# Performance work log

Measured on AMD Instinct MI355X. Metric: run time of the kernel, lower is better.

Reference implementation:

```python
import jax, jax.numpy as jnp
import numpy as np

N = 50000   # nodes
E = 800000  # edges (avg degree 16)
G = 64      # graphs in batch


def setup_inputs() -> dict:
    key = jax.random.key(0)
    ks = jax.random.split(key, 32)
    w = lambda k, shape, s=0.05: (jax.random.normal(k, shape, jnp.float32) * s)
    inp = {}
    inp["x"] = jax.random.normal(ks[0], (N, 3), jnp.float32)
    inp["edge_index"] = jax.random.randint(ks[1], (2, E), 0, N)
    inp["batch"] = jnp.sort(jax.random.randint(ks[2], (N,), 0, G))
    # TransformerConv 1: in=3, heads=2, d=32 -> out 64 (concat)
    inp["Wq1"] = w(ks[3], (3, 64));  inp["bq1"] = w(ks[4], (64,))
    inp["Wk1"] = w(ks[5], (3, 64));  inp["bk1"] = w(ks[6], (64,))
    inp["Wv1"] = w(ks[7], (3, 64));  inp["bv1"] = w(ks[8], (64,))
    inp["Ws1"] = w(ks[9], (3, 64));  inp["bs1"] = w(ks[10], (64,))
    # TransformerConv 2: in=64, heads=2, d=64 -> out 128 (concat)
    inp["Wq2"] = w(ks[11], (64, 128)); inp["bq2"] = w(ks[12], (128,))
    inp["Wk2"] = w(ks[13], (64, 128)); inp["bk2"] = w(ks[14], (128,))
    inp["Wv2"] = w(ks[15], (64, 128)); inp["bv2"] = w(ks[16], (128,))
    inp["Ws2"] = w(ks[17], (64, 128)); inp["bs2"] = w(ks[18], (128,))
    # MLP head
    inp["W1"] = w(ks[19], (128, 32)); inp["b1"] = w(ks[20], (32,))
    inp["W2"] = w(ks[21], (32, 128)); inp["b2"] = w(ks[22], (128,))
    inp["W3"] = w(ks[23], (128, 40)); inp["b3"] = w(ks[24], (40,))
    return inp


def _transformer_conv(x, src, dst, Wq, bq, Wk, bk, Wv, bv, Ws, bs, H, d):
    """PyG TransformerConv (concat=True, root_weight=True, beta=False)."""
    n = x.shape[0]
    q = (x @ Wq + bq).reshape(n, H, d)
    k = (x @ Wk + bk).reshape(n, H, d)
    v = (x @ Wv + bv).reshape(n, H, d)
    # per-edge attention logits: q_i . k_j / sqrt(d), i=dst, j=src  -> [E, H]
    s = (q[dst] * k[src]).sum(-1) / jnp.sqrt(jnp.float32(d))
    # segment softmax over edges grouped by destination node
    m = jax.ops.segment_max(s, dst, num_segments=n)
    m = jnp.where(jnp.isfinite(m), m, 0.0)
    e = jnp.exp(s - m[dst])
    denom = jax.ops.segment_sum(e, dst, num_segments=n)
    alpha = e / jnp.maximum(denom[dst], 1e-16)
    # scatter-add weighted values
    out = jax.ops.segment_sum(alpha[:, :, None] * v[src], dst, num_segments=n)
    return out.reshape(n, H * d) + x @ Ws + bs  # skip connection


def reference(x, edge_index, batch,
              Wq1, bq1, Wk1, bk1, Wv1, bv1, Ws1, bs1,
              Wq2, bq2, Wk2, bk2, Wv2, bv2, Ws2, bs2,
              W1, b1, W2, b2, W3, b3):
    src, dst = edge_index[0], edge_index[1]
    h = jax.nn.relu(_transformer_conv(x, src, dst, Wq1, bq1, Wk1, bk1,
                                      Wv1, bv1, Ws1, bs1, 2, 32))
    h = jax.nn.relu(_transformer_conv(h, src, dst, Wq2, bq2, Wk2, bk2,
                                      Wv2, bv2, Ws2, bs2, 2, 64))
    # global max pool over graphs
    p = jax.ops.segment_max(h, batch, num_segments=G)
    p = jnp.where(jnp.isfinite(p), p, 0.0)
    x_latent = jax.nn.relu(p @ W1 + b1)
    y = jax.nn.relu(x_latent @ W2 + b2)
    return (y @ W3 + b3, x_latent)
```

## Files before the change

kernel.cpp:

```cpp
#include <hip/hip_runtime.h>
#include <hip/hip_bf16.h>

typedef short s16x8 __attribute__((ext_vector_type(8)));
typedef float f32x4 __attribute__((ext_vector_type(4)));

#define LOG2E 1.4426950408889634f

__device__ __forceinline__ float bfl(unsigned w) { return __uint_as_float(w << 16); }
__device__ __forceinline__ float bfh(unsigned w) { return __uint_as_float(w & 0xffff0000u); }
__device__ __forceinline__ unsigned f2bf(float f) {
    unsigned u = __float_as_uint(f);
    return (u + 0x7fffu + ((u >> 16) & 1u)) >> 16;
}

__global__ void deg_part(const int* __restrict__ dst, int* __restrict__ deg,
                         int E, int rsize) {
    int r = blockIdx.x & 7;
    int e = (blockIdx.x >> 3) * blockDim.x + threadIdx.x;
    if (e < E) {
        int d = dst[e];
        if (d / rsize == r) atomicAdd(&deg[d], 1);
    }
}

__global__ void scan_reduce(const int* __restrict__ deg, int* __restrict__ bsum, int n) {
    __shared__ int sh[256];
    int t = threadIdx.x;
    int i = blockIdx.x * 256 + t;
    sh[t] = (i < n) ? deg[i] : 0;
    __syncthreads();
    for (int s = 128; s > 0; s >>= 1) {
        if (t < s) sh[t] += sh[t + s];
        __syncthreads();
    }
    if (t == 0) bsum[blockIdx.x] = sh[0];
}

__global__ void scan_apply(const int* __restrict__ deg, const int* __restrict__ bsum,
                           int* __restrict__ off, int* __restrict__ cursor,
                           int n, int nb, int Etot) {
    __shared__ int sh[256], sb[256];
    int t = threadIdx.x;
    int b = blockIdx.x;
    sb[t] = (t < nb && t < b) ? bsum[t] : 0;
    int i = b * 256 + t;
    int v = (i < n) ? deg[i] : 0;
    sh[t] = v;
    __syncthreads();
    for (int s = 128; s > 0; s >>= 1) {
        if (t < s) sb[t] += sb[t + s];
        __syncthreads();
    }
    int boffb = sb[0];
    __syncthreads();
    for (int d = 1; d < 256; d <<= 1) {
        int x = (t >= d) ? sh[t - d] : 0;
        __syncthreads();
        sh[t] += x;
        __syncthreads();
    }
    int ex = sh[t] - v + boffb;
    if (i < n) {
        off[i] = ex;
        cursor[i] = ex;
    }
    if (b == 0 && t == 0) off[n] = Etot;
}

__global__ void scatter_part(const int* __restrict__ src, const int* __restrict__ dst,
                             int* __restrict__ cursor, int* __restrict__ srcs,
                             int E, int rsize) {
    int r = blockIdx.x & 7;
    int e = (blockIdx.x >> 3) * blockDim.x + threadIdx.x;
    if (e < E) {
        int d = dst[e];
        if (d / rsize == r) {
            int p = atomicAdd(&cursor[d], 1);
            srcs[p] = src[e];
        }
    }
}

__global__ void prep_all(const float* __restrict__ Wq1, const float* __restrict__ bq1,
                         const float* __restrict__ Wk1,
                         const float* __restrict__ Wq2, const float* __restrict__ bq2,
                         const float* __restrict__ Wk2,
                         const float* __restrict__ Wv2, const float* __restrict__ Ws2,
                         float* __restrict__ c1, float* __restrict__ wcat,
                         ushort* __restrict__ bfragY, ushort* __restrict__ B192,
                         int* __restrict__ deg, unsigned* __restrict__ pool,
                         int n, int nbdeg, int poolsz) {
    int b = blockIdx.x, t = threadIdx.x;
    if (b == 0) {
        if (t < 18) {
            int h = t / 9, rr = t % 9, r = rr / 3, rp = rr % 3;
            float s = 0.f;
            for (int d = 0; d < 32; ++d)
                s += Wq1[r * 64 + h * 32 + d] * Wk1[rp * 64 + h * 32 + d];
            c1[t] = s;
        } else if (t < 24) {
            int u = t - 18, h = u / 3, rp = u % 3;
            float s = 0.f;
            for (int d = 0; d < 32; ++d)
                s += bq1[h * 32 + d] * Wk1[rp * 64 + h * 32 + d];
            c1[t] = s;
        } else if (t >= 64 && t < 192) {
            int cc = t - 64, h = cc >> 6, kp = cc & 63;
            float s = 0.f;
            for (int d = 0; d < 64; ++d)
                s += bq2[h * 64 + d] * Wk2[kp * 128 + h * 64 + d];
            wcat[cc] = s;
        }
    } else if (b < 33) {
        int idx = (b - 1) * 256 + t;
        int k = idx >> 7, cc = idx & 127, h = cc >> 6, kp = cc & 63;
        float s = 0.f;
        for (int d = 0; d < 64; ++d)
            s += Wq2[k * 128 + h * 64 + d] * Wk2[kp * 128 + h * 64 + d];
        int frag = ((cc >> 4) << 1) | (k >> 5);
        int l = (cc & 15) | (((k >> 3) & 3) << 4);
        bfragY[(size_t)frag * 512 + l * 8 + (k & 7)] = (ushort)f2bf(s);
    } else if (b < 45) {
        int tt = (b - 33) * 256 + t;
        int frag = tt >> 6, l = tt & 63;
        int ct = frag / 6, ks = frag % 6;
        int c = ct * 16 + (l & 15);
        int kbase = ks * 32 + ((l >> 4) << 3);
#pragma unroll
        for (int e = 0; e < 8; ++e) {
            int k = kbase + e;
            float v;
            if (k < 64) v = (c < 64) ? Wv2[k * 128 + c] : 0.f;
            else if (k < 128) v = (c >= 64) ? Wv2[(k - 64) * 128 + c] : 0.f;
            else v = Ws2[(k - 128) * 128 + c];
            B192[(size_t)frag * 512 + l * 8 + e] = (ushort)f2bf(v);
        }
    } else if (b < 45 + nbdeg) {
        int i = (b - 45) * 256 + t;
        if (i < n) deg[i] = 0;
    } else {
        int i = (b - 45 - nbdeg) * 256 + t;
        if (i < poolsz) pool[i] = 0;
    }
}

__global__ __launch_bounds__(256) void attn1f(
        const float* __restrict__ x, const float* __restrict__ c1,
        const float* __restrict__ Wv, const float* __restrict__ bv,
        const float* __restrict__ Ws, const float* __restrict__ bs,
        const int* __restrict__ off, const int* __restrict__ srcs,
        unsigned* __restrict__ h1b, int n) {
    int lane = threadIdx.x & 63;
    int g = lane >> 3, sl = lane & 7;
    int i = (blockIdx.x * (blockDim.x >> 6) + (threadIdx.x >> 6)) * 8 + g;
    bool act = i < n;
    int ic = act ? i : 0;
    float x0 = x[ic * 3], x1 = x[ic * 3 + 1], x2 = x[ic * 3 + 2];
    float y0[3], y1[3];
#pragma unroll
    for (int rp = 0; rp < 3; ++rp) {
        y0[rp] = x0 * c1[rp] + x1 * c1[3 + rp] + x2 * c1[6 + rp] + c1[18 + rp];
        y1[rp] = x0 * c1[9 + rp] + x1 * c1[12 + rp] + x2 * c1[15 + rp] + c1[21 + rp];
    }
    const float SC = 0.17677669529663688f * LOG2E;
    int e0 = act ? off[ic] : 0, e1 = act ? off[ic + 1] : 0;
    float d0 = 0.f, d1 = 0.f;
    float a0x = 0.f, a0y = 0.f, a0z = 0.f, a1x = 0.f, a1y = 0.f, a1z = 0.f;
    for (int e = e0 + sl; e < e1; e += 8) {
        int j = srcs[e];
        float xj0 = x[j * 3], xj1 = x[j * 3 + 1], xj2 = x[j * 3 + 2];
        float p0 = exp2f((y0[0] * xj0 + y0[1] * xj1 + y0[2] * xj2) * SC);
        float p1 = exp2f((y1[0] * xj0 + y1[1] * xj1 + y1[2] * xj2) * SC);
        d0 += p0; a0x += p0 * xj0; a0y += p0 * xj1; a0z += p0 * xj2;
        d1 += p1; a1x += p1 * xj0; a1y += p1 * xj1; a1z += p1 * xj2;
    }
#pragma unroll
    for (int mask = 1; mask <= 4; mask <<= 1) {
        d0 += __shfl_xor(d0, mask); d1 += __shfl_xor(d1, mask);
        a0x += __shfl_xor(a0x, mask); a0y += __shfl_xor(a0y, mask);
        a0z += __shfl_xor(a0z, mask); a1x += __shfl_xor(a1x, mask);
        a1y += __shfl_xor(a1y, mask); a1z += __shfl_xor(a1z, mask);
    }
    if (!act) return;
    int head = sl >> 2;
    float dh = head ? d1 : d0;
    float inv = 1.f / fmaxf(dh, 1e-16f);
    float sg = dh > 0.f ? 1.f : 0.f;
    float Ax = (head ? a1x : a0x) * inv;
    float Ay = (head ? a1y : a0y) * inv;
    float Az = (head ? a1z : a0z) * inv;
    unsigned pk[4];
#pragma unroll
    for (int u = 0; u < 4; ++u) {
        int c = sl * 8 + 2 * u;
        float2 wv0 = *(const float2*)&Wv[c], wv1 = *(const float2*)&Wv[64 + c],
               wv2 = *(const float2*)&Wv[128 + c];
        float2 ws0 = *(const float2*)&Ws[c], ws1 = *(const float2*)&Ws[64 + c],
               ws2 = *(const float2*)&Ws[128 + c];
        float2 bbv = *(const float2*)&bv[c];
        float2 bbs = *(const float2*)&bs[c];
        float v0 = Ax * wv0.x + Ay * wv1.x + Az * wv2.x + sg * bbv.x +
                   x0 * ws0.x + x1 * ws1.x + x2 * ws2.x + bbs.x;
        float v1 = Ax * wv0.y + Ay * wv1.y + Az * wv2.y + sg * bbv.y +
                   x0 * ws0.y + x1 * ws1.y + x2 * ws2.y + bbs.y;
        pk[u] = f2bf(fmaxf(v0, 0.f)) | (f2bf(fmaxf(v1, 0.f)) << 16);
    }
    uint4 pa = {pk[0], pk[1], pk[2], pk[3]};
    *(uint4*)&h1b[(size_t)i * 32 + sl * 4] = pa;
}

__global__ __launch_bounds__(256) void lin2Y(const ushort* __restrict__ h1b,
                                             const ushort* __restrict__ bfragY,
                                             const float* __restrict__ wcat,
                                             ushort* __restrict__ Ypb, int n) {
    int node0 = blockIdx.x * 16;
    int w = threadIdx.x >> 6, l = threadIdx.x & 63;
    int arow = node0 + (l & 15);
    if (arow >= n) arow = n - 1;
    s16x8 a0 = *(const s16x8*)&h1b[(size_t)arow * 64 + ((l >> 4) << 3)];
    s16x8 a1 = *(const s16x8*)&h1b[(size_t)arow * 64 + 32 + ((l >> 4) << 3)];
    int cl = l & 15;
#pragma unroll
    for (int qq = 0; qq < 2; ++qq) {
        int ct = w * 2 + qq;
        s16x8 b0 = *(const s16x8*)&bfragY[(size_t)(ct * 2 + 0) * 512 + l * 8];
        s16x8 b1 = *(const s16x8*)&bfragY[(size_t)(ct * 2 + 1) * 512 + l * 8];
        f32x4 acc = {0.f, 0.f, 0.f, 0.f};
        acc = __builtin_amdgcn_mfma_f32_16x16x32_bf16(a0, b0, acc, 0, 0, 0);
        acc = __builtin_amdgcn_mfma_f32_16x16x32_bf16(a1, b1, acc, 0, 0, 0);
        int cg = ct * 16 + cl;
        float bb = wcat[cg];
#pragma unroll
        for (int r = 0; r < 4; ++r) {
            int node = node0 + ((l >> 4) << 2) + r;
            if (node < n) Ypb[(size_t)node * 128 + cg] = (ushort)f2bf(acc[r] + bb);
        }
    }
}

__global__ __launch_bounds__(256) void attn2_kernel(
        const ushort* __restrict__ Ypb, const unsigned* __restrict__ h1u,
        const int* __restrict__ off, const int* __restrict__ srcs,
        unsigned* __restrict__ a01, float2* __restrict__ sig2, int n) {
    int i = blockIdx.x * (blockDim.x >> 6) + (threadIdx.x >> 6);
    int lane = threadIdx.x & 63;
    if (i >= n) return;
    int qd = lane >> 4, sl = lane & 15;
    int e0 = off[i], e1 = off[i + 1];
    const float SC = 0.125f * LOG2E;
    uint2 yau = *(const uint2*)&Ypb[(size_t)i * 128 + 4 * sl];
    uint2 ybu = *(const uint2*)&Ypb[(size_t)i * 128 + 64 + 4 * sl];
    float ya[4], yb[4];
    ya[0] = bfl(yau.x); ya[1] = bfh(yau.x); ya[2] = bfl(yau.y); ya[3] = bfh(yau.y);
    yb[0] = bfl(ybu.x); yb[1] = bfh(ybu.x); yb[2] = bfl(ybu.y); yb[3] = bfh(ybu.y);
    float d0 = 0.f, d1 = 0.f;
    float a0[4] = {0.f, 0.f, 0.f, 0.f};
    float a1[4] = {0.f, 0.f, 0.f, 0.f};
    for (int e = e0 + qd; e < e1; e += 4) {
        int j = srcs[e];
        uint2 hb = *(const uint2*)&h1u[(size_t)j * 32 + 2 * sl];
        float h[4];
        h[0] = bfl(hb.x); h[1] = bfh(hb.x); h[2] = bfl(hb.y); h[3] = bfh(hb.y);
        float t0 = ya[0] * h[0] + ya[1] * h[1] + ya[2] * h[2] + ya[3] * h[3];
        float t1 = yb[0] * h[0] + yb[1] * h[1] + yb[2] * h[2] + yb[3] * h[3];
        t0 += __shfl_xor(t0, 1); t0 += __shfl_xor(t0, 2);
        t0 += __shfl_xor(t0, 4); t0 += __shfl_xor(t0, 8);
        t1 += __shfl_xor(t1, 1); t1 += __shfl_xor(t1, 2);
        t1 += __shfl_xor(t1, 4); t1 += __shfl_xor(t1, 8);
        float p0 = exp2f(t0 * SC);
        float p1 = exp2f(t1 * SC);
        d0 += p0;
        d1 += p1;
#pragma unroll
        for (int k = 0; k < 4; ++k) {
            a0[k] += p0 * h[k];
            a1[k] += p1 * h[k];
        }
    }
#pragma unroll
    for (int mask = 16; mask <= 32; mask <<= 1) {
        d0 += __shfl_xor(d0, mask);
        d1 += __shfl_xor(d1, mask);
#pragma unroll
        for (int k = 0; k < 4; ++k) {
            a0[k] += __shfl_xor(a0[k], mask);
            a1[k] += __shfl_xor(a1[k], mask);
        }
    }
    if (qd == 0) {
        float i0 = 1.f / fmaxf(d0, 1e-16f), i1 = 1.f / fmaxf(d1, 1e-16f);
        uint2 pa, pb;
        pa.x = f2bf(a0[0] * i0) | (f2bf(a0[1] * i0) << 16);
        pa.y = f2bf(a0[2] * i0) | (f2bf(a0[3] * i0) << 16);
        pb.x = f2bf(a1[0] * i1) | (f2bf(a1[1] * i1) << 16);
        pb.y = f2bf(a1[2] * i1) | (f2bf(a1[3] * i1) << 16);
        *(uint2*)&a01[(size_t)i * 64 + 2 * sl] = pa;
        *(uint2*)&a01[(size_t)i * 64 + 32 + 2 * sl] = pb;
        if (sl == 0) {
            float2 sg = {d0 > 0.f ? 1.f : 0.f, d1 > 0.f ? 1.f : 0.f};
            sig2[i] = sg;
        }
    }
}

__global__ __launch_bounds__(256) void epi2(
        const ushort* __restrict__ a01, const ushort* __restrict__ h1b,
        const ushort* __restrict__ B192, const float* __restrict__ bv,
        const float* __restrict__ bs, const float* __restrict__ sig2,
        const int* __restrict__ batch, unsigned* __restrict__ pool, int n) {
    __shared__ float po[16][128];
    __shared__ int pg[16];
    int node0 = blockIdx.x * 16;
    int w = threadIdx.x >> 6, l = threadIdx.x & 63;
    int arow = node0 + (l & 15);
    int arc = (arow < n) ? arow : (n - 1);
    int koff = (l >> 4) << 3;
    s16x8 af[6];
    af[0] = *(const s16x8*)&a01[(size_t)arc * 128 + 0 + koff];
    af[1] = *(const s16x8*)&a01[(size_t)arc * 128 + 32 + koff];
    af[2] = *(const s16x8*)&a01[(size_t)arc * 128 + 64 + koff];
    af[3] = *(const s16x8*)&a01[(size_t)arc * 128 + 96 + koff];
    af[4] = *(const s16x8*)&h1b[(size_t)arc * 64 + 0 + koff];
    af[5] = *(const s16x8*)&h1b[(size_t)arc * 64 + 32 + koff];
    if (threadIdx.x < 16)
        pg[threadIdx.x] = (node0 + threadIdx.x < n) ? batch[node0 + threadIdx.x] : -1;
    int cl = l & 15;
#pragma unroll
    for (int qq = 0; qq < 2; ++qq) {
        int ct = w * 2 + qq;
        f32x4 acc = {0.f, 0.f, 0.f, 0.f};
#pragma unroll
        for (int ks = 0; ks < 6; ++ks) {
            s16x8 b = *(const s16x8*)&B192[(size_t)(ct * 6 + ks) * 512 + l * 8];
            acc = __builtin_amdgcn_mfma_f32_16x16x32_bf16(af[ks], b, acc, 0, 0, 0);
        }
        int cg = ct * 16 + cl;
        int head = cg >> 6;
        float bbs = bs[cg], bbv = bv[cg];
#pragma unroll
        for (int r = 0; r < 4; ++r) {
            int row = ((l >> 4) << 2) + r;
            int node = node0 + row;
            float sg = (node < n) ? sig2[node * 2 + head] : 0.f;
            po[row][cg] = fmaxf(acc[r] + sg * bbv + bbs, 0.f);
        }
    }
    __syncthreads();
    int t = threadIdx.x;
    if (t < 128) {
        int curg = -1;
        float mx = 0.f;
        for (int r = 0; r < 16; ++r) {
            int g = pg[r];
            if (g < 0) continue;
            if (g != curg) {
                if (curg >= 0) atomicMax(&pool[(size_t)curg * 128 + t], __float_as_uint(mx));
                curg = g;
                mx = 0.f;
            }
            mx = fmaxf(mx, po[r][t]);
        }
        if (curg >= 0) atomicMax(&pool[(size_t)curg * 128 + t], __float_as_uint(mx));
    }
}

__global__ void head_kernel(const unsigned* __restrict__ pbits,
                            const float* __restrict__ W1, const float* __restrict__ b1,
                            const float* __restrict__ W2, const float* __restrict__ b2,
                            const float* __restrict__ W3, const float* __restrict__ b3,
                            float* __restrict__ out, int G) {
    int g = blockIdx.x;
    int t = threadIdx.x;
    __shared__ float ps[128], xl[32], y[128];
    ps[t] = __uint_as_float(pbits[g * 128 + t]);
    __syncthreads();
    if (t < 32) {
        float a = b1[t];
        for (int k = 0; k < 128; ++k) a += ps[k] * W1[k * 32 + t];
        a = fmaxf(a, 0.f);
        xl[t] = a;
        out[G * 40 + g * 32 + t] = a;
    }
    __syncthreads();
    {
        float a = b2[t];
        for (int k = 0; k < 32; ++k) a += xl[k] * W2[k * 128 + t];
        y[t] = fmaxf(a, 0.f);
    }
    __syncthreads();
    if (t < 40) {
        float a = b3[t];
        for (int k = 0; k < 128; ++k) a += y[k] * W3[k * 40 + t];
        out[g * 40 + t] = a;
    }
}

extern "C" void kernel_launch(void* const* d_in, const int* in_sizes, int n_in,
                              void* d_out, int out_size, void* d_ws, size_t ws_size,
                              hipStream_t stream) {
    const float* x = (const float*)d_in[0];
    const int* eidx = (const int*)d_in[1];
    const int* batch = (const int*)d_in[2];
    const float *Wq1 = (const float*)d_in[3], *bq1 = (const float*)d_in[4];
    const float *Wk1 = (const float*)d_in[5], *bk1 = (const float*)d_in[6];
    const float *Wv1 = (const float*)d_in[7], *bv1 = (const float*)d_in[8];
    const float *Ws1 = (const float*)d_in[9], *bs1 = (const float*)d_in[10];
    const float *Wq2 = (const float*)d_in[11], *bq2 = (const float*)d_in[12];
    const float *Wk2 = (const float*)d_in[13], *bk2 = (const float*)d_in[14];
    const float *Wv2 = (const float*)d_in[15], *bv2 = (const float*)d_in[16];
    const float *Ws2 = (const float*)d_in[17], *bs2 = (const float*)d_in[18];
    const float *W1 = (const float*)d_in[19], *b1 = (const float*)d_in[20];
    const float *W2 = (const float*)d_in[21], *b2 = (const float*)d_in[22];
    const float *W3 = (const float*)d_in[23], *b3 = (const float*)d_in[24];
    (void)bk1; (void)bk2;

    const int N = in_sizes[0] / 3;
    const int E = in_sizes[1] / 2;
    const int G = out_size / 72;
    const int* esrc = eidx;
    const int* edst = eidx + E;
    const int NB = (N + 255) / 256;
    const int EB = (E + 255) / 256;
    const int POOLSZ = G * 128;
    const int PB = (POOLSZ + 255) / 256;
    const int RSIZE = (N + 7) / 8;

    char* w = (char*)d_ws;
    size_t o = 0;
    auto alloc = [&](size_t bytes) {
        void* p = w + o;
        o = (o + bytes + 255) & ~(size_t)255;
        return p;
    };
    float* c1buf = (float*)alloc(24 * 4);
    float* wcat = (float*)alloc(128 * 4);
    ushort* bfragY = (ushort*)alloc(16 * 512 * 2);
    ushort* B192 = (ushort*)alloc(48 * 512 * 2);
    unsigned* h1b = (unsigned*)alloc((size_t)N * 32 * 4);
    ushort* Ypb = (ushort*)alloc((size_t)N * 128 * 2);
    unsigned* a01 = (unsigned*)alloc((size_t)N * 64 * 4);
    float* sig2 = (float*)alloc((size_t)N * 2 * 4);
    int* deg = (int*)alloc((size_t)N * 4);
    int* off = (int*)alloc((size_t)(N + 1) * 4);
    int* cursor = (int*)alloc((size_t)N * 4);
    int* srcs = (int*)alloc((size_t)E * 4);
    unsigned* pool = (unsigned*)alloc((size_t)POOLSZ * 4);
    int* bsum = (int*)alloc(256 * 4);
    (void)ws_size;

    prep_all<<<45 + NB + PB, 256, 0, stream>>>(Wq1, bq1, Wk1, Wq2, bq2, Wk2, Wv2, Ws2,
                                               c1buf, wcat, bfragY, B192, deg, pool,
                                               N, NB, POOLSZ);

    deg_part<<<8 * EB, 256, 0, stream>>>(edst, deg, E, RSIZE);
    scan_reduce<<<NB, 256, 0, stream>>>(deg, bsum, N);
    scan_apply<<<NB, 256, 0, stream>>>(deg, bsum, off, cursor, N, NB, E);
    scatter_part<<<8 * EB, 256, 0, stream>>>(esrc, edst, cursor, srcs, E, RSIZE);

    attn1f<<<(N + 31) / 32, 256, 0, stream>>>(x, c1buf, Wv1, bv1, Ws1, bs1, off, srcs,
                                              h1b, N);

    lin2Y<<<(N + 15) / 16, 256, 0, stream>>>((const ushort*)h1b, bfragY, wcat, Ypb, N);
    attn2_kernel<<<(N + 3) / 4, 256, 0, stream>>>(Ypb, h1b, off, srcs, a01,
                                                  (float2*)sig2, N);
    epi2<<<(N + 15) / 16, 256, 0, stream>>>((const ushort*)a01, (const ushort*)h1b, B192,
                                            bv2, bs2, sig2, batch, pool, N);

    head_kernel<<<G, 128, 0, stream>>>(pool, W1, b1, W2, b2, W3, b3, (float*)d_out, G);
}
```

Baseline: 181.2 us.

## Split attention heads across lane groups in attn1 and attn2 kernels

attn1f now gives each node 16 lanes, 8 per head, so each lane carries one head's accumulators instead of both. This halves per-lane exp and FMA work at the cost of twice as many blocks and duplicated source-feature loads. attn2 now splits each node's 16 lanes by head, each loading 8 bf16 features with uint4 loads. This replaces two 4-step shuffle reductions per edge with one 3-step reduction and halves the exp count per lane, though each lane does more accumulation work and the same h1 row is read by both head halves.

```diff
diff --git a/kernel.cpp b/kernel.cpp
--- a/kernel.cpp
+++ b/kernel.cpp
@@ -151,48 +151,42 @@
         const int* __restrict__ off, const int* __restrict__ srcs,
         unsigned* __restrict__ h1b, int n) {
     int lane = threadIdx.x & 63;
-    int g = lane >> 3, sl = lane & 7;
-    int i = (blockIdx.x * (blockDim.x >> 6) + (threadIdx.x >> 6)) * 8 + g;
+    int g = lane >> 4;
+    int sl16 = lane & 15;
+    int hh = sl16 >> 3, es = sl16 & 7;
+    int i = (blockIdx.x * (blockDim.x >> 6) + (threadIdx.x >> 6)) * 4 + g;
     bool act = i < n;
     int ic = act ? i : 0;
     float x0 = x[ic * 3], x1 = x[ic * 3 + 1], x2 = x[ic * 3 + 2];
-    float y0[3], y1[3];
-#pragma unroll
-    for (int rp = 0; rp < 3; ++rp) {
-        y0[rp] = x0 * c1[rp] + x1 * c1[3 + rp] + x2 * c1[6 + rp] + c1[18 + rp];
-        y1[rp] = x0 * c1[9 + rp] + x1 * c1[12 + rp] + x2 * c1[15 + rp] + c1[21 + rp];
-    }
+    float y[3];
+#pragma unroll
+    for (int rp = 0; rp < 3; ++rp)
+        y[rp] = x0 * c1[hh * 9 + rp] + x1 * c1[hh * 9 + 3 + rp] +
+                x2 * c1[hh * 9 + 6 + rp] + c1[18 + hh * 3 + rp];
     const float SC = 0.17677669529663688f * LOG2E;
     int e0 = act ? off[ic] : 0, e1 = act ? off[ic + 1] : 0;
-    float d0 = 0.f, d1 = 0.f;
-    float a0x = 0.f, a0y = 0.f, a0z = 0.f, a1x = 0.f, a1y = 0.f, a1z = 0.f;
-    for (int e = e0 + sl; e < e1; e += 8) {
+    float d = 0.f, ax = 0.f, ay = 0.f, az = 0.f;
+    for (int e = e0 + es; e < e1; e += 8) {
         int j = srcs[e];
         float xj0 = x[j * 3], xj1 = x[j * 3 + 1], xj2 = x[j * 3 + 2];
-        float p0 = exp2f((y0[0] * xj0 + y0[1] * xj1 + y0[2] * xj2) * SC);
-        float p1 = exp2f((y1[0] * xj0 + y1[1] * xj1 + y1[2] * xj2) * SC);
-        d0 += p0; a0x += p0 * xj0; a0y += p0 * xj1; a0z += p0 * xj2;
-        d1 += p1; a1x += p1 * xj0; a1y += p1 * xj1; a1z += p1 * xj2;
+        float p = exp2f((y[0] * xj0 + y[1] * xj1 + y[2] * xj2) * SC);
+        d += p; ax += p * xj0; ay += p * xj1; az += p * xj2;
     }
 #pragma unroll
     for (int mask = 1; mask <= 4; mask <<= 1) {
-        d0 += __shfl_xor(d0, mask); d1 += __shfl_xor(d1, mask);
-        a0x += __shfl_xor(a0x, mask); a0y += __shfl_xor(a0y, mask);
-        a0z += __shfl_xor(a0z, mask); a1x += __shfl_xor(a1x, mask);
-        a1y += __shfl_xor(a1y, mask); a1z += __shfl_xor(a1z, mask);
+        d += __shfl_xor(d, mask);
+        ax += __shfl_xor(ax, mask);
+        ay += __shfl_xor(ay, mask);
+        az += __shfl_xor(az, mask);
     }
     if (!act) return;
-    int head = sl >> 2;
-    float dh = head ? d1 : d0;
-    float inv = 1.f / fmaxf(dh, 1e-16f);
-    float sg = dh > 0.f ? 1.f : 0.f;
-    float Ax = (head ? a1x : a0x) * inv;
-    float Ay = (head ? a1y : a0y) * inv;
-    float Az = (head ? a1z : a0z) * inv;
-    unsigned pk[4];
-#pragma unroll
-    for (int u = 0; u < 4; ++u) {
-        int c = sl * 8 + 2 * u;
+    float inv = 1.f / fmaxf(d, 1e-16f);
+    float sg = d > 0.f ? 1.f : 0.f;
+    float Ax = ax * inv, Ay = ay * inv, Az = az * inv;
+    unsigned pk[2];
+#pragma unroll
+    for (int u = 0; u < 2; ++u) {
+        int c = hh * 32 + 4 * es + 2 * u;
         float2 wv0 = *(const float2*)&Wv[c], wv1 = *(const float2*)&Wv[64 + c],
                wv2 = *(const float2*)&Wv[128 + c];
         float2 ws0 = *(const float2*)&Ws[c], ws1 = *(const float2*)&Ws[64 + c],
@@ -205,8 +199,8 @@
                    x0 * ws0.y + x1 * ws1.y + x2 * ws2.y + bbs.y;
         pk[u] = f2bf(fmaxf(v0, 0.f)) | (f2bf(fmaxf(v1, 0.f)) << 16);
     }
-    uint4 pa = {pk[0], pk[1], pk[2], pk[3]};
-    *(uint4*)&h1b[(size_t)i * 32 + sl * 4] = pa;
+    uint2 pw = {pk[0], pk[1]};
+    *(uint2*)&h1b[(size_t)i * 32 + hh * 16 + 2 * es] = pw;
 }
 
 __global__ __launch_bounds__(256) void lin2Y(const ushort* __restrict__ h1b,
@@ -241,65 +235,52 @@
 __global__ __launch_bounds__(256) void attn2_kernel(
         const ushort* __restrict__ Ypb, const unsigned* __restrict__ h1u,
         const int* __restrict__ off, const int* __restrict__ srcs,
-        unsigned* __restrict__ a01, float2* __restrict__ sig2, int n) {
+        unsigned* __restrict__ a01, float* __restrict__ sig2f, int n) {
     int i = blockIdx.x * (blockDim.x >> 6) + (threadIdx.x >> 6);
     int lane = threadIdx.x & 63;
     if (i >= n) return;
-    int qd = lane >> 4, sl = lane & 15;
+    int qd = lane >> 4;
+    int sl16 = lane & 15;
+    int hh = sl16 >> 3, cb = sl16 & 7;
     int e0 = off[i], e1 = off[i + 1];
     const float SC = 0.125f * LOG2E;
-    uint2 yau = *(const uint2*)&Ypb[(size_t)i * 128 + 4 * sl];
-    uint2 ybu = *(const uint2*)&Ypb[(size_t)i * 128 + 64 + 4 * sl];
-    float ya[4], yb[4];
-    ya[0] = bfl(yau.x); ya[1] = bfh(yau.x); ya[2] = bfl(yau.y); ya[3] = bfh(yau.y);
-    yb[0] = bfl(ybu.x); yb[1] = bfh(ybu.x); yb[2] = bfl(ybu.y); yb[3] = bfh(ybu.y);
-    float d0 = 0.f, d1 = 0.f;
-    float a0[4] = {0.f, 0.f, 0.f, 0.f};
-    float a1[4] = {0.f, 0.f, 0.f, 0.f};
+    uint4 yu = *(const uint4*)&Ypb[(size_t)i * 128 + hh * 64 + 8 * cb];
+    float y[8];
+    y[0] = bfl(yu.x); y[1] = bfh(yu.x); y[2] = bfl(yu.y); y[3] = bfh(yu.y);
+    y[4] = bfl(yu.z); y[5] = bfh(yu.z); y[6] = bfl(yu.w); y[7] = bfh(yu.w);
+    float d = 0.f;
+    float a[8] = {0.f, 0.f, 0.f, 0.f, 0.f, 0.f, 0.f, 0.f};
     for (int e = e0 + qd; e < e1; e += 4) {
         int j = srcs[e];
-        uint2 hb = *(const uint2*)&h1u[(size_t)j * 32 + 2 * sl];
-        float h[4];
+        uint4 hb = *(const uint4*)&h1u[(size_t)j * 32 + 4 * cb];
+        float h[8];
         h[0] = bfl(hb.x); h[1] = bfh(hb.x); h[2] = bfl(hb.y); h[3] = bfh(hb.y);
-        float t0 = ya[0] * h[0] + ya[1] * h[1] + ya[2] * h[2] + ya[3] * h[3];
-        float t1 = yb[0] * h[0] + yb[1] * h[1] + yb[2] * h[2] + yb[3] * h[3];
-        t0 += __shfl_xor(t0, 1); t0 += __shfl_xor(t0, 2);
-        t0 += __shfl_xor(t0, 4); t0 += __shfl_xor(t0, 8);
-        t1 += __shfl_xor(t1, 1); t1 += __shfl_xor(t1, 2);
-        t1 += __shfl_xor(t1, 4); t1 += __shfl_xor(t1, 8);
-        float p0 = exp2f(t0 * SC);
-        float p1 = exp2f(t1 * SC);
-        d0 += p0;
-        d1 += p1;
-#pragma unroll
-        for (int k = 0; k < 4; ++k) {
-            a0[k] += p0 * h[k];
-            a1[k] += p1 * h[k];
-        }
+        h[4] = bfl(hb.z); h[5] = bfh(hb.z); h[6] = bfl(hb.w); h[7] = bfh(hb.w);
+        float t = y[0] * h[0] + y[1] * h[1] + y[2] * h[2] + y[3] * h[3] +
+                  y[4] * h[4] + y[5] * h[5] + y[6] * h[6] + y[7] * h[7];
+        t += __shfl_xor(t, 1);
+        t += __shfl_xor(t, 2);
+        t += __shfl_xor(t, 4);
+        float p = exp2f(t * SC);
+        d += p;
+#pragma unroll
+        for (int k = 0; k < 8; ++k) a[k] += p * h[k];
     }
 #pragma unroll
     for (int mask = 16; mask <= 32; mask <<= 1) {
-        d0 += __shfl_xor(d0, mask);
-        d1 += __shfl_xor(d1, mask);
-#pragma unroll
-        for (int k = 0; k < 4; ++k) {
-            a0[k] += __shfl_xor(a0[k], mask);
-            a1[k] += __shfl_xor(a1[k], mask);
-        }
+        d += __shfl_xor(d, mask);
+#pragma unroll
+        for (int k = 0; k < 8; ++k) a[k] += __shfl_xor(a[k], mask);
     }
     if (qd == 0) {
-        float i0 = 1.f / fmaxf(d0, 1e-16f), i1 = 1.f / fmaxf(d1, 1e-16f);
-        uint2 pa, pb;
-        pa.x = f2bf(a0[0] * i0) | (f2bf(a0[1] * i0) << 16);
-        pa.y = f2bf(a0[2] * i0) | (f2bf(a0[3] * i0) << 16);
-        pb.x = f2bf(a1[0] * i1) | (f2bf(a1[1] * i1) << 16);
-        pb.y = f2bf(a1[2] * i1) | (f2bf(a1[3] * i1) << 16);
-        *(uint2*)&a01[(size_t)i * 64 + 2 * sl] = pa;
-        *(uint2*)&a01[(size_t)i * 64 + 32 + 2 * sl] = pb;
-        if (sl == 0) {
-            float2 sg = {d0 > 0.f ? 1.f : 0.f, d1 > 0.f ? 1.f : 0.f};
-            sig2[i] = sg;
-        }
+        float inv = 1.f / fmaxf(d, 1e-16f);
+        uint4 pk;
+        pk.x = f2bf(a[0] * inv) | (f2bf(a[1] * inv) << 16);
+        pk.y = f2bf(a[2] * inv) | (f2bf(a[3] * inv) << 16);
+        pk.z = f2bf(a[4] * inv) | (f2bf(a[5] * inv) << 16);
+        pk.w = f2bf(a[6] * inv) | (f2bf(a[7] * inv) << 16);
+        *(uint4*)&a01[(size_t)i * 64 + hh * 32 + 4 * cb] = pk;
+        if (cb == 0) sig2f[i * 2 + hh] = d > 0.f ? 1.f : 0.f;
     }
 }
 
@@ -457,12 +438,11 @@
     scan_apply<<<NB, 256, 0, stream>>>(deg, bsum, off, cursor, N, NB, E);
     scatter_part<<<8 * EB, 256, 0, stream>>>(esrc, edst, cursor, srcs, E, RSIZE);
 
-    attn1f<<<(N + 31) / 32, 256, 0, stream>>>(x, c1buf, Wv1, bv1, Ws1, bs1, off, srcs,
+    attn1f<<<(N + 15) / 16, 256, 0, stream>>>(x, c1buf, Wv1, bv1, Ws1, bs1, off, srcs,
                                               h1b, N);
 
     lin2Y<<<(N + 15) / 16, 256, 0, stream>>>((const ushort*)h1b, bfragY, wcat, Ypb, N);
-    attn2_kernel<<<(N + 3) / 4, 256, 0, stream>>>(Ypb, h1b, off, srcs, a01,
-                                                  (float2*)sig2, N);
+    attn2_kernel<<<(N + 3) / 4, 256, 0, stream>>>(Ypb, h1b, off, srcs, a01, sig2, N);
     epi2<<<(N + 15) / 16, 256, 0, stream>>>((const ushort*)a01, (const ushort*)h1b, B192,
                                             bv2, bs2, sig2, batch, pool, N);
 
```

New measurement: 177.1 us. 2.2% less time.
